# Kernel optimization log

Measured on AMD Instinct MI355X. Metric: run time of the kernel, lower is better.

The kernel has to match this reference:

```python
import jax, jax.numpy as jnp
import numpy as np

D_MODEL = 1024
NUM_HEADS = 16
HEAD_DIM = D_MODEL // NUM_HEADS
SEQ_LEN = 2048
BATCH = 2


def setup_inputs() -> dict:
    key = jax.random.key(0)
    ks = jax.random.split(key, 8)
    s = 1.0 / np.sqrt(D_MODEL)
    x = jax.random.normal(ks[0], (BATCH, SEQ_LEN, D_MODEL), jnp.float32)
    Wq = jax.random.normal(ks[1], (D_MODEL, D_MODEL), jnp.float32) * s
    Wk = jax.random.normal(ks[2], (D_MODEL, D_MODEL), jnp.float32) * s
    Wv = jax.random.normal(ks[3], (D_MODEL, D_MODEL), jnp.float32) * s
    Wo = jax.random.normal(ks[4], (D_MODEL, D_MODEL), jnp.float32) * s
    bq = jnp.zeros((D_MODEL,), jnp.float32)
    bk = jnp.zeros((D_MODEL,), jnp.float32)
    bv = jnp.zeros((D_MODEL,), jnp.float32)
    bo = jnp.zeros((D_MODEL,), jnp.float32)
    pos_embed = jax.random.normal(ks[5], (SEQ_LEN, HEAD_DIM), jnp.float32) * (1.0 / np.sqrt(HEAD_DIM))
    alpha = jnp.ones((NUM_HEADS, 1, 1), jnp.float32)
    beta = jnp.zeros((NUM_HEADS, 1, 1), jnp.float32)
    mask = jnp.ones((BATCH, SEQ_LEN), jnp.int32)
    return {"x": x, "mask": mask, "Wq": Wq, "bq": bq, "Wk": Wk, "bk": bk,
            "Wv": Wv, "bv": bv, "Wo": Wo, "bo": bo,
            "pos_embed": pos_embed, "alpha": alpha, "beta": beta}


def reference(x, mask, Wq, bq, Wk, bk, Wv, bv, Wo, bo, pos_embed, alpha, beta):
    B, S, _ = x.shape
    H, Dh = NUM_HEADS, HEAD_DIM
    # projections (torch Linear: x @ W^T + b), reshape to [B,H,S,Dh]
    def proj(W, b):
        return (x @ W.T + b).reshape(B, S, H, Dh).transpose(0, 2, 1, 3)
    q = proj(Wq, bq)
    k = proj(Wk, bk)
    v = proj(Wv, bv)
    # content scores [B,H,S,S]
    content = jnp.einsum('bhqd,bhkd->bhqk', q, k) / np.sqrt(Dh).astype(np.float32)
    # position scores [S,S] -> broadcast; combined with per-head alpha/beta
    pe = pos_embed[:S]
    pos_attn = pe @ pe.T  # [S,S]
    scores = content + (alpha * pos_attn[None] + beta)[None]  # [B,H,S,S]
    # mask: [B,S] broadcast over heads and query positions (key-side mask)
    scores = jnp.where(mask[:, None, None, :] == 0, -jnp.inf, scores)
    probs = jax.nn.softmax(scores, axis=-1)
    out = jnp.einsum('bhqk,bhkd->bhqd', probs, v)  # [B,H,S,Dh]
    out = out.transpose(0, 2, 1, 3).reshape(B, S, H * Dh)
    return out @ Wo.T + bo
```

## Files before the change

kernel.cpp:

```cpp
#include <hip/hip_runtime.h>

#define BATCH 2
#define SEQ   2048
#define NH    16
#define DH    64
#define DA    128
#define DM    1024
#define MTOT  (BATCH*SEQ)

typedef _Float16 f16x8 __attribute__((ext_vector_type(8)));
typedef _Float16 f16x4 __attribute__((ext_vector_type(4)));
typedef float    f32x4 __attribute__((ext_vector_type(4)));
typedef float    f32x16 __attribute__((ext_vector_type(16)));

#define LOG2E 1.44269504088896340736f

#define OFF_X16 0u
#define OFF_WQ  8388608u
#define OFF_WK  10485760u
#define OFF_WV  12582912u
#define OFF_WO  14680064u
#define OFF_QA  16777216u
#define OFF_KA  33554432u
#define OFF_VT  50331648u
#define OFF_AO  58720256u

__device__ __forceinline__ void gload_lds16(const _Float16* g, _Float16* l) {
  __builtin_amdgcn_global_load_lds(
      (const __attribute__((address_space(1))) unsigned int*)g,
      (__attribute__((address_space(3))) unsigned int*)l, 16, 0, 0);
}

__device__ __forceinline__ float fexp2(float x) {
  float r;
  asm("v_exp_f32 %0, %1" : "=v"(r) : "v"(x));
  return r;
}

__device__ __forceinline__ unsigned pk2(float a, float b) {
  auto v = __builtin_amdgcn_cvt_pkrtz(a, b);
  return *(unsigned*)&v;
}

__global__ __launch_bounds__(256) void cvt_all(
    const float* __restrict__ x,  const float* __restrict__ wq,
    const float* __restrict__ wk, const float* __restrict__ wv,
    const float* __restrict__ wo, _Float16* __restrict__ dst)
{
  int i = blockIdx.x * 256 + threadIdx.x;
  const float* src;
  if (i < 524288) {
    src = x + (size_t)i * 8;
  } else {
    int j = i - 524288;
    int wi = j >> 17;
    const float* w = (wi == 0) ? wq : ((wi == 1) ? wk : ((wi == 2) ? wv : wo));
    src = w + (size_t)(j & 131071) * 8;
  }
  float4 a = ((const float4*)src)[0];
  float4 c = ((const float4*)src)[1];
  f16x8 hv;
  hv[0]=(_Float16)a.x; hv[1]=(_Float16)a.y; hv[2]=(_Float16)a.z; hv[3]=(_Float16)a.w;
  hv[4]=(_Float16)c.x; hv[5]=(_Float16)c.y; hv[6]=(_Float16)c.z; hv[7]=(_Float16)c.w;
  *(f16x8*)(dst + (size_t)i * 8) = hv;
}

__global__ __launch_bounds__(256) void fill_pe(
    const float* __restrict__ pe, const float* __restrict__ alpha,
    _Float16* __restrict__ Qa, _Float16* __restrict__ Ka)
{
  int idx = blockIdx.x * 256 + threadIdx.x;
  int c8 = idx & 7;
  int s  = (idx >> 3) & 2047;
  int h  = (idx >> 14) & 15;
  int b  = idx >> 18;
  const float4* p4 = (const float4*)(pe + s * 64 + c8 * 8);
  float4 a = p4[0], c = p4[1];
  float al = alpha[h] * LOG2E;
  f16x8 hk, hq;
  hk[0]=(_Float16)a.x; hk[1]=(_Float16)a.y; hk[2]=(_Float16)a.z; hk[3]=(_Float16)a.w;
  hk[4]=(_Float16)c.x; hk[5]=(_Float16)c.y; hk[6]=(_Float16)c.z; hk[7]=(_Float16)c.w;
  hq[0]=(_Float16)(al*a.x); hq[1]=(_Float16)(al*a.y); hq[2]=(_Float16)(al*a.z); hq[3]=(_Float16)(al*a.w);
  hq[4]=(_Float16)(al*c.x); hq[5]=(_Float16)(al*c.y); hq[6]=(_Float16)(al*c.z); hq[7]=(_Float16)(al*c.w);
  size_t o = ((size_t)((b * NH + h) * SEQ + s)) * DA + 64 + c8 * 8;
  *(f16x8*)&Qa[o] = hq;
  *(f16x8*)&Ka[o] = hk;
}

template<int MODE>
__global__ __launch_bounds__(256) void gemm_nt(
    const _Float16* __restrict__ A,
    const _Float16* __restrict__ W0, const _Float16* __restrict__ W1,
    const _Float16* __restrict__ W2,
    const float* __restrict__ b0, const float* __restrict__ b1,
    const float* __restrict__ b2,
    _Float16* __restrict__ Qa, _Float16* __restrict__ Ka,
    _Float16* __restrict__ Vt, float* __restrict__ Out)
{
  __shared__ _Float16 As[128 * 64];
  __shared__ _Float16 Bs[128 * 64];
  const int tid = threadIdx.x;
  const int w = tid >> 6, lane = tid & 63;
  const int g = lane >> 4, l16 = lane & 15;
  const int wm = w >> 1, wn = w & 1;

  int nb_all = blockIdx.x;
  int mblk = blockIdx.y;
  const _Float16* Bp; const float* biasp;
  int which = 0, nblk = nb_all;
  if (MODE == 0) {
    which = nb_all >> 3; nblk = nb_all & 7;
    Bp = (which == 0) ? W0 : ((which == 1) ? W1 : W2);
    biasp = (which == 0) ? b0 : ((which == 1) ? b1 : b2);
  } else {
    Bp = W0; biasp = b0;
  }

  f32x4 zero4 = {0.f, 0.f, 0.f, 0.f};
  f32x4 acc[4][4];
  #pragma unroll
  for (int mb = 0; mb < 4; ++mb)
    #pragma unroll
    for (int nb = 0; nb < 4; ++nb) acc[mb][nb] = zero4;

  const _Float16* Abase = A  + (size_t)mblk * 128 * DM;
  const _Float16* Bbase = Bp + (size_t)nblk * 128 * DM;

  for (int kt = 0; kt < DM / 64; ++kt) {
    __syncthreads();
    #pragma unroll
    for (int ii = 0; ii < 4; ++ii) {
      int i = w * 4 + ii;
      int rt = i * 8 + (lane >> 3);
      int cg = (lane & 7) ^ (rt & 7);
      gload_lds16(Abase + (size_t)rt * DM + kt * 64 + cg * 8, &As[i * 512]);
    }
    #pragma unroll
    for (int ii = 0; ii < 4; ++ii) {
      int i = w * 4 + ii;
      int rt = i * 8 + (lane >> 3);
      int cg = (lane & 7) ^ (rt & 7);
      gload_lds16(Bbase + (size_t)rt * DM + kt * 64 + cg * 8, &Bs[i * 512]);
    }
    __syncthreads();
    #pragma unroll
    for (int ks = 0; ks < 2; ++ks) {
      f16x8 av[4], bv[4];
      #pragma unroll
      for (int mb = 0; mb < 4; ++mb) {
        int rt = wm * 64 + mb * 16 + l16;
        av[mb] = *(const f16x8*)&As[rt * 64 + (((ks * 4 + g) ^ (rt & 7)) * 8)];
      }
      #pragma unroll
      for (int nb = 0; nb < 4; ++nb) {
        int rt = wn * 64 + nb * 16 + l16;
        bv[nb] = *(const f16x8*)&Bs[rt * 64 + (((ks * 4 + g) ^ (rt & 7)) * 8)];
      }
      #pragma unroll
      for (int mb = 0; mb < 4; ++mb)
        #pragma unroll
        for (int nb = 0; nb < 4; ++nb)
          acc[mb][nb] = __builtin_amdgcn_mfma_f32_16x16x32_f16(
              av[mb], bv[nb], acc[mb][nb], 0, 0, 0);
    }
  }

  #pragma unroll
  for (int nb = 0; nb < 4; ++nb) {
    int n = nblk * 128 + wn * 64 + nb * 16 + l16;
    float bias = biasp[n];
    #pragma unroll
    for (int mb = 0; mb < 4; ++mb) {
      int m0 = mblk * 128 + wm * 64 + mb * 16 + g * 4;
      if (MODE == 0) {
        int hh = n >> 6, dd = n & 63;
        if (which == 2) {
          int bb = m0 >> 11, ss = m0 & 2047;
          f16x4 hv;
          #pragma unroll
          for (int r = 0; r < 4; ++r) hv[r] = (_Float16)(acc[mb][nb][r] + bias);
          *(f16x4*)&Vt[((size_t)((bb * NH + hh) * DH + dd)) * SEQ + ss] = hv;
        } else {
          #pragma unroll
          for (int r = 0; r < 4; ++r) {
            int m = m0 + r; int bb = m >> 11, ss = m & 2047;
            size_t o = ((size_t)((bb * NH + hh) * SEQ + ss)) * DA + dd;
            if (which == 0) Qa[o] = (_Float16)((acc[mb][nb][r] + bias) * (0.125f * LOG2E));
            else            Ka[o] = (_Float16)(acc[mb][nb][r] + bias);
          }
        }
      } else {
        #pragma unroll
        for (int r = 0; r < 4; ++r)
          Out[(size_t)(m0 + r) * DM + n] = acc[mb][nb][r] + bias;
      }
    }
  }
}

__global__ __launch_bounds__(256, 3) void flash_attn(
    const _Float16* __restrict__ Qa, const _Float16* __restrict__ Ka,
    const _Float16* __restrict__ Vt, const int* __restrict__ mask,
    _Float16* __restrict__ AO)
{
  __shared__ _Float16 Ks[2][64 * 128];
  __shared__ _Float16 Vs[2][64 * 64];
  const int tid = threadIdx.x;
  const int w = tid >> 6, lane = tid & 63;
  const int l32 = lane & 31, hi = lane >> 5;

  int bid = blockIdx.x;
  int work = (bid & 7) * 64 + (bid >> 3);
  const int qt = work & 15;
  const int bh = work >> 4;
  const int h = bh & 15, b = bh >> 4;

  const _Float16* qbase = Qa + ((size_t)(bh * SEQ) + qt * 128 + w * 32) * DA;
  f16x8 qf[8];
  #pragma unroll
  for (int c16 = 0; c16 < 8; ++c16)
    qf[c16] = *(const f16x8*)&qbase[l32 * DA + c16 * 16 + hi * 8];

  f32x16 acco[2];
  #pragma unroll
  for (int db = 0; db < 2; ++db)
    #pragma unroll
    for (int r = 0; r < 16; ++r) acco[db][r] = 0.f;
  float mrun = -3.0e38f, lrun = 0.f;

  const _Float16* kbase = Ka + (size_t)bh * SEQ * DA;
  const _Float16* vbase = Vt + (size_t)bh * DH * SEQ;
  const int* mbase = mask + b * SEQ;

  int allm = 1;
  #pragma unroll 8
  for (int t = 0; t < SEQ / 64; ++t) allm &= (mbase[t * 64 + lane] != 0);
  const bool maskclean = __all(allm);

  auto STAGE = [&](int buf, int kt) {
    #pragma unroll
    for (int ii = 0; ii < 4; ++ii) {
      int i = ii * 256 + tid;
      int rt = i >> 4, c = i & 15;
      int cg = c ^ (rt & 7);
      gload_lds16(kbase + (size_t)(kt * 64 + rt) * DA + cg * 8, &Ks[buf][i * 8]);
    }
    #pragma unroll
    for (int ii = 0; ii < 2; ++ii) {
      int i = ii * 256 + tid;
      int rt = i >> 3, c = i & 7;
      int cg = c ^ (rt & 7);
      gload_lds16(vbase + (size_t)rt * SEQ + kt * 64 + cg * 8, &Vs[buf][i * 8]);
    }
  };

  STAGE(0, 0);
  int cur = 0;
  for (int kt = 0; kt < SEQ / 64; ++kt) {
    asm volatile("s_waitcnt lgkmcnt(0)" ::: "memory");
    __builtin_amdgcn_s_barrier();
    asm volatile("" ::: "memory");
    if (kt + 1 < SEQ / 64) {
      STAGE(cur ^ 1, kt + 1);
      asm volatile("s_waitcnt vmcnt(6)" ::: "memory");
    } else {
      asm volatile("s_waitcnt vmcnt(0)" ::: "memory");
    }
    __builtin_amdgcn_s_barrier();
    asm volatile("" ::: "memory");

    f32x16 sfr[2];
    __builtin_amdgcn_s_setprio(1);
    #pragma unroll
    for (int kb = 0; kb < 2; ++kb) {
      f32x16 s;
      #pragma unroll
      for (int r = 0; r < 16; ++r) s[r] = 0.f;
      int rt = kb * 32 + l32;
      #pragma unroll
      for (int c16 = 0; c16 < 8; ++c16) {
        int ch = (2 * c16 + hi) ^ (rt & 7);
        f16x8 kf = *(const f16x8*)&Ks[cur][rt * 128 + ch * 8];
        s = __builtin_amdgcn_mfma_f32_32x32x16_f16(kf, qf[c16], s, 0, 0, 0);
      }
      sfr[kb] = s;
    }
    __builtin_amdgcn_s_setprio(0);

    if (!maskclean) {
      #pragma unroll
      for (int kb = 0; kb < 2; ++kb)
        #pragma unroll
        for (int r = 0; r < 16; ++r) {
          int key = kt * 64 + kb * 32 + (r & 3) + 8 * (r >> 2) + 4 * hi;
          if (mbase[key] == 0) sfr[kb][r] = -3.0e38f;
        }
    }

    float mx = sfr[0][0];
    #pragma unroll
    for (int kb = 0; kb < 2; ++kb)
      #pragma unroll
      for (int r = 0; r < 16; ++r) mx = fmaxf(mx, sfr[kb][r]);
    mx = fmaxf(mx, __shfl_xor(mx, 32));

    const bool rescale = !__all(mx <= mrun + 8.0f);
    float mnew = mrun, scale = 1.0f;
    if (rescale) {
      mnew = fmaxf(mrun, mx);
      scale = fexp2(mrun - mnew);
    }
    float rsum = 0.f;
    unsigned pk[2][4][2];
    #pragma unroll
    for (int kb = 0; kb < 2; ++kb)
      #pragma unroll
      for (int rq = 0; rq < 4; ++rq) {
        float p0 = fexp2(sfr[kb][rq * 4 + 0] - mnew);
        float p1 = fexp2(sfr[kb][rq * 4 + 1] - mnew);
        float p2 = fexp2(sfr[kb][rq * 4 + 2] - mnew);
        float p3 = fexp2(sfr[kb][rq * 4 + 3] - mnew);
        rsum += (p0 + p1) + (p2 + p3);
        pk[kb][rq][0] = pk2(p0, p1);
        pk[kb][rq][1] = pk2(p2, p3);
      }
    rsum += __shfl_xor(rsum, 32);
    if (rescale) {
      lrun = lrun * scale + rsum;
      mrun = mnew;
      #pragma unroll
      for (int db = 0; db < 2; ++db)
        #pragma unroll
        for (int r = 0; r < 16; ++r) acco[db][r] *= scale;
    } else {
      lrun += rsum;
    }

    __builtin_amdgcn_s_setprio(1);
    #pragma unroll
    for (int c = 0; c < 4; ++c) {
      const int kb = c >> 1, c2 = c & 1;
      unsigned X0 = pk[kb][2 * c2][0],     X1 = pk[kb][2 * c2][1];
      unsigned Y0 = pk[kb][2 * c2 + 1][0], Y1 = pk[kb][2 * c2 + 1][1];
      asm("v_permlane32_swap_b32 %0, %1" : "+v"(X0), "+v"(Y0));
      asm("v_permlane32_swap_b32 %0, %1" : "+v"(X1), "+v"(Y1));
      union { unsigned u[4]; f16x8 v; } pu;
      pu.u[0] = X0; pu.u[1] = X1; pu.u[2] = Y0; pu.u[3] = Y1;
      #pragma unroll
      for (int db = 0; db < 2; ++db) {
        int row = db * 32 + l32;
        int ch = (2 * c + hi) ^ (row & 7);
        f16x8 vf = *(const f16x8*)&Vs[cur][row * 64 + ch * 8];
        acco[db] = __builtin_amdgcn_mfma_f32_32x32x16_f16(vf, pu.v, acco[db], 0, 0, 0);
      }
    }
    __builtin_amdgcn_s_setprio(0);
    cur ^= 1;
  }

  float inv = 1.0f / lrun;
  int sg = qt * 128 + w * 32 + l32;
  _Float16* aobase = AO + ((size_t)(b * SEQ + sg)) * DM + h * DH;
  #pragma unroll
  for (int db = 0; db < 2; ++db)
    #pragma unroll
    for (int rq = 0; rq < 4; ++rq) {
      f16x4 o;
      #pragma unroll
      for (int j = 0; j < 4; ++j) o[j] = (_Float16)(acco[db][rq * 4 + j] * inv);
      *(f16x4*)&aobase[db * 32 + rq * 8 + hi * 4] = o;
    }
}

extern "C" void kernel_launch(void* const* d_in, const int* in_sizes, int n_in,
                              void* d_out, int out_size, void* d_ws, size_t ws_size,
                              hipStream_t stream) {
  const float* x     = (const float*)d_in[0];
  const int*   mask  = (const int*)  d_in[1];
  const float* Wq    = (const float*)d_in[2];
  const float* bq    = (const float*)d_in[3];
  const float* Wk    = (const float*)d_in[4];
  const float* bk    = (const float*)d_in[5];
  const float* Wv    = (const float*)d_in[6];
  const float* bv    = (const float*)d_in[7];
  const float* Wo    = (const float*)d_in[8];
  const float* bo    = (const float*)d_in[9];
  const float* pe    = (const float*)d_in[10];
  const float* alpha = (const float*)d_in[11];

  char* ws = (char*)d_ws;
  _Float16* x16 = (_Float16*)(ws + OFF_X16);
  _Float16* wq6 = (_Float16*)(ws + OFF_WQ);
  _Float16* wk6 = (_Float16*)(ws + OFF_WK);
  _Float16* wv6 = (_Float16*)(ws + OFF_WV);
  _Float16* wo6 = (_Float16*)(ws + OFF_WO);
  _Float16* Qa  = (_Float16*)(ws + OFF_QA);
  _Float16* Ka  = (_Float16*)(ws + OFF_KA);
  _Float16* Vt  = (_Float16*)(ws + OFF_VT);
  _Float16* AO  = (_Float16*)(ws + OFF_AO);
  float* out = (float*)d_out;

  cvt_all<<<4096, 256, 0, stream>>>(x, Wq, Wk, Wv, Wo, x16);
  fill_pe<<<2048, 256, 0, stream>>>(pe, alpha, Qa, Ka);
  gemm_nt<0><<<dim3(24, 32), 256, 0, stream>>>(x16, wq6, wk6, wv6, bq, bk, bv,
                                               Qa, Ka, Vt, nullptr);
  flash_attn<<<512, 256, 0, stream>>>(Qa, Ka, Vt, mask, AO);
  gemm_nt<1><<<dim3(8, 32), 256, 0, stream>>>(AO, wo6, nullptr, nullptr, bo,
                                              nullptr, nullptr, nullptr, nullptr,
                                              nullptr, out);
}
```

Measured before the change: 149.4 us.

## Split online softmax into per-32-key sub-blocks interleaved with PV MFMAs

Restructures the attention inner loop so the max/rescale/exp/PV-MFMA sequence runs separately for each 32-key half of the 64-key tile, instead of once over the whole tile. This lets the softmax VALU work of one half overlap with the MFMAs of the other and lowers register pressure, since only one half's packed probabilities are live at a time. In exchange there are twice as many cross-lane reductions and rescale checks per tile, so the accumulator may be rescaled more often.

Measured after the change: 154.7 us. +3.5%, slower.

```diff
diff --git a/kernel.cpp b/kernel.cpp
--- a/kernel.cpp
+++ b/kernel.cpp
@@ -287,74 +287,68 @@
     }
     __builtin_amdgcn_s_setprio(0);
 
-    if (!maskclean) {
-      #pragma unroll
-      for (int kb = 0; kb < 2; ++kb)
+    #pragma unroll
+    for (int kb = 0; kb < 2; ++kb) {
+      if (!maskclean) {
         #pragma unroll
         for (int r = 0; r < 16; ++r) {
           int key = kt * 64 + kb * 32 + (r & 3) + 8 * (r >> 2) + 4 * hi;
           if (mbase[key] == 0) sfr[kb][r] = -3.0e38f;
         }
-    }
-
-    float mx = sfr[0][0];
-    #pragma unroll
-    for (int kb = 0; kb < 2; ++kb)
-      #pragma unroll
-      for (int r = 0; r < 16; ++r) mx = fmaxf(mx, sfr[kb][r]);
-    mx = fmaxf(mx, __shfl_xor(mx, 32));
-
-    const bool rescale = !__all(mx <= mrun + 8.0f);
-    float mnew = mrun, scale = 1.0f;
-    if (rescale) {
-      mnew = fmaxf(mrun, mx);
-      scale = fexp2(mrun - mnew);
-    }
-    float rsum = 0.f;
-    unsigned pk[2][4][2];
-    #pragma unroll
-    for (int kb = 0; kb < 2; ++kb)
+      }
+      float t0 = fmaxf(fmaxf(sfr[kb][0], sfr[kb][1]), fmaxf(sfr[kb][2], sfr[kb][3]));
+      float t1 = fmaxf(fmaxf(sfr[kb][4], sfr[kb][5]), fmaxf(sfr[kb][6], sfr[kb][7]));
+      float t2 = fmaxf(fmaxf(sfr[kb][8], sfr[kb][9]), fmaxf(sfr[kb][10], sfr[kb][11]));
+      float t3 = fmaxf(fmaxf(sfr[kb][12], sfr[kb][13]), fmaxf(sfr[kb][14], sfr[kb][15]));
+      float mx = fmaxf(fmaxf(t0, t1), fmaxf(t2, t3));
+      mx = fmaxf(mx, __shfl_xor(mx, 32));
+
+      const bool rescale = !__all(mx <= mrun + 8.0f);
+      if (rescale) {
+        float mnew = fmaxf(mrun, mx);
+        float scale = fexp2(mrun - mnew);
+        lrun *= scale;
+        #pragma unroll
+        for (int db = 0; db < 2; ++db)
+          #pragma unroll
+          for (int r = 0; r < 16; ++r) acco[db][r] *= scale;
+        mrun = mnew;
+      }
+      float rsum = 0.f;
+      unsigned pk[4][2];
       #pragma unroll
       for (int rq = 0; rq < 4; ++rq) {
-        float p0 = fexp2(sfr[kb][rq * 4 + 0] - mnew);
-        float p1 = fexp2(sfr[kb][rq * 4 + 1] - mnew);
-        float p2 = fexp2(sfr[kb][rq * 4 + 2] - mnew);
-        float p3 = fexp2(sfr[kb][rq * 4 + 3] - mnew);
+        float p0 = fexp2(sfr[kb][rq * 4 + 0] - mrun);
+        float p1 = fexp2(sfr[kb][rq * 4 + 1] - mrun);
+        float p2 = fexp2(sfr[kb][rq * 4 + 2] - mrun);
+        float p3 = fexp2(sfr[kb][rq * 4 + 3] - mrun);
         rsum += (p0 + p1) + (p2 + p3);
-        pk[kb][rq][0] = pk2(p0, p1);
-        pk[kb][rq][1] = pk2(p2, p3);
-      }
-    rsum += __shfl_xor(rsum, 32);
-    if (rescale) {
-      lrun = lrun * scale + rsum;
-      mrun = mnew;
-      #pragma unroll
-      for (int db = 0; db < 2; ++db)
+        pk[rq][0] = pk2(p0, p1);
+        pk[rq][1] = pk2(p2, p3);
+      }
+      rsum += __shfl_xor(rsum, 32);
+      lrun += rsum;
+
+      __builtin_amdgcn_s_setprio(1);
+      #pragma unroll
+      for (int c2 = 0; c2 < 2; ++c2) {
+        unsigned X0 = pk[2 * c2][0],     X1 = pk[2 * c2][1];
+        unsigned Y0 = pk[2 * c2 + 1][0], Y1 = pk[2 * c2 + 1][1];
+        asm("v_permlane32_swap_b32 %0, %1" : "+v"(X0), "+v"(Y0));
+        asm("v_permlane32_swap_b32 %0, %1" : "+v"(X1), "+v"(Y1));
+        union { unsigned u[4]; f16x8 v; } pu;
+        pu.u[0] = X0; pu.u[1] = X1; pu.u[2] = Y0; pu.u[3] = Y1;
+        const int c = kb * 2 + c2;
         #pragma unroll
-        for (int r = 0; r < 16; ++r) acco[db][r] *= scale;
-    } else {
-      lrun += rsum;
-    }
-
-    __builtin_amdgcn_s_setprio(1);
-    #pragma unroll
-    for (int c = 0; c < 4; ++c) {
-      const int kb = c >> 1, c2 = c & 1;
-      unsigned X0 = pk[kb][2 * c2][0],     X1 = pk[kb][2 * c2][1];
-      unsigned Y0 = pk[kb][2 * c2 + 1][0], Y1 = pk[kb][2 * c2 + 1][1];
-      asm("v_permlane32_swap_b32 %0, %1" : "+v"(X0), "+v"(Y0));
-      asm("v_permlane32_swap_b32 %0, %1" : "+v"(X1), "+v"(Y1));
-      union { unsigned u[4]; f16x8 v; } pu;
-      pu.u[0] = X0; pu.u[1] = X1; pu.u[2] = Y0; pu.u[3] = Y1;
-      #pragma unroll
-      for (int db = 0; db < 2; ++db) {
-        int row = db * 32 + l32;
-        int ch = (2 * c + hi) ^ (row & 7);
-        f16x8 vf = *(const f16x8*)&Vs[cur][row * 64 + ch * 8];
-        acco[db] = __builtin_amdgcn_mfma_f32_32x32x16_f16(vf, pu.v, acco[db], 0, 0, 0);
-      }
-    }
-    __builtin_amdgcn_s_setprio(0);
+        for (int db = 0; db < 2; ++db) {
+          int row = db * 32 + l32;
+          int ch = (2 * c + hi) ^ (row & 7);
+          f16x8 vf = *(const f16x8*)&Vs[cur][row * 64 + ch * 8];
+          acco[db] = __builtin_amdgcn_mfma_f32_32x32x16_f16(vf, pu.v, acco[db], 0, 0, 0);
+        }
+      }
+      __builtin_amdgcn_s_setprio(0);
+    }
     cur ^= 1;
   }
 
```

## Split attention keys across two halves and merge partials in a combine kernel

Applied to the files above, without the earlier changes.

The flash-attention kernel now gives each 512-thread block 256 queries (8 waves) over one half of the keys. It writes normalized fp16 partial outputs plus per-row (max, sum) statistics, and a new combine_halves kernel merges the two halves with log-sum-exp weights. The wider block shares each staged K/V tile across twice as many query waves, which halves global-to-LDS staging per query, and each block loop is half as long. In exchange it adds an extra kernel launch, extra partial-output traffic, and reuses dead workspace regions (x16, the Wq area) as scratch. It also tightens launch bounds to (512,4), which may force register spills given the large per-thread accumulator and fragment state.

Measured after the change: 156.7 us. 4.9% more time.

```diff
diff --git a/kernel.cpp b/kernel.cpp
--- a/kernel.cpp
+++ b/kernel.cpp
@@ -198,10 +198,11 @@
   }
 }
 
-__global__ __launch_bounds__(256, 3) void flash_attn(
+__global__ __launch_bounds__(512, 4) void flash_attn(
     const _Float16* __restrict__ Qa, const _Float16* __restrict__ Ka,
     const _Float16* __restrict__ Vt, const int* __restrict__ mask,
-    _Float16* __restrict__ AO)
+    _Float16* __restrict__ pp0, _Float16* __restrict__ pp1,
+    float2* __restrict__ Ml)
 {
   __shared__ _Float16 Ks[2][64 * 128];
   __shared__ _Float16 Vs[2][64 * 64];
@@ -211,11 +212,12 @@
 
   int bid = blockIdx.x;
   int work = (bid & 7) * 64 + (bid >> 3);
-  const int qt = work & 15;
-  const int bh = work >> 4;
+  const int qt   = work & 7;
+  const int half = (work >> 3) & 1;
+  const int bh   = work >> 4;
   const int h = bh & 15, b = bh >> 4;
 
-  const _Float16* qbase = Qa + ((size_t)(bh * SEQ) + qt * 128 + w * 32) * DA;
+  const _Float16* qbase = Qa + ((size_t)(bh * SEQ) + qt * 256 + w * 32) * DA;
   f16x8 qf[8];
   #pragma unroll
   for (int c16 = 0; c16 < 8; ++c16)
@@ -226,28 +228,27 @@
   for (int db = 0; db < 2; ++db)
     #pragma unroll
     for (int r = 0; r < 16; ++r) acco[db][r] = 0.f;
-  float mrun = -3.0e38f, lrun = 0.f;
-
-  const _Float16* kbase = Ka + (size_t)bh * SEQ * DA;
-  const _Float16* vbase = Vt + (size_t)bh * DH * SEQ;
-  const int* mbase = mask + b * SEQ;
+  float mrun = -1.0e30f, lrun = 0.f;
+
+  const _Float16* kbase = Ka + (size_t)bh * SEQ * DA + (size_t)half * 1024 * DA;
+  const _Float16* vbase = Vt + (size_t)bh * DH * SEQ + half * 1024;
+  const int* mbase = mask + b * SEQ + half * 1024;
 
   int allm = 1;
   #pragma unroll 8
-  for (int t = 0; t < SEQ / 64; ++t) allm &= (mbase[t * 64 + lane] != 0);
+  for (int t = 0; t < 16; ++t) allm &= (mbase[t * 64 + lane] != 0);
   const bool maskclean = __all(allm);
 
   auto STAGE = [&](int buf, int kt) {
     #pragma unroll
-    for (int ii = 0; ii < 4; ++ii) {
-      int i = ii * 256 + tid;
+    for (int ii = 0; ii < 2; ++ii) {
+      int i = ii * 512 + tid;
       int rt = i >> 4, c = i & 15;
       int cg = c ^ (rt & 7);
       gload_lds16(kbase + (size_t)(kt * 64 + rt) * DA + cg * 8, &Ks[buf][i * 8]);
     }
-    #pragma unroll
-    for (int ii = 0; ii < 2; ++ii) {
-      int i = ii * 256 + tid;
+    {
+      int i = tid;
       int rt = i >> 3, c = i & 7;
       int cg = c ^ (rt & 7);
       gload_lds16(vbase + (size_t)rt * SEQ + kt * 64 + cg * 8, &Vs[buf][i * 8]);
@@ -256,13 +257,13 @@
 
   STAGE(0, 0);
   int cur = 0;
-  for (int kt = 0; kt < SEQ / 64; ++kt) {
+  for (int kt = 0; kt < 16; ++kt) {
     asm volatile("s_waitcnt lgkmcnt(0)" ::: "memory");
     __builtin_amdgcn_s_barrier();
     asm volatile("" ::: "memory");
-    if (kt + 1 < SEQ / 64) {
+    if (kt + 1 < 16) {
       STAGE(cur ^ 1, kt + 1);
-      asm volatile("s_waitcnt vmcnt(6)" ::: "memory");
+      asm volatile("s_waitcnt vmcnt(3)" ::: "memory");
     } else {
       asm volatile("s_waitcnt vmcnt(0)" ::: "memory");
     }
@@ -297,11 +298,16 @@
         }
     }
 
-    float mx = sfr[0][0];
-    #pragma unroll
-    for (int kb = 0; kb < 2; ++kb)
-      #pragma unroll
-      for (int r = 0; r < 16; ++r) mx = fmaxf(mx, sfr[kb][r]);
+    float t0 = fmaxf(fmaxf(sfr[0][0], sfr[0][1]), fmaxf(sfr[0][2], sfr[0][3]));
+    float t1 = fmaxf(fmaxf(sfr[0][4], sfr[0][5]), fmaxf(sfr[0][6], sfr[0][7]));
+    float t2 = fmaxf(fmaxf(sfr[0][8], sfr[0][9]), fmaxf(sfr[0][10], sfr[0][11]));
+    float t3 = fmaxf(fmaxf(sfr[0][12], sfr[0][13]), fmaxf(sfr[0][14], sfr[0][15]));
+    float u0 = fmaxf(fmaxf(sfr[1][0], sfr[1][1]), fmaxf(sfr[1][2], sfr[1][3]));
+    float u1 = fmaxf(fmaxf(sfr[1][4], sfr[1][5]), fmaxf(sfr[1][6], sfr[1][7]));
+    float u2 = fmaxf(fmaxf(sfr[1][8], sfr[1][9]), fmaxf(sfr[1][10], sfr[1][11]));
+    float u3 = fmaxf(fmaxf(sfr[1][12], sfr[1][13]), fmaxf(sfr[1][14], sfr[1][15]));
+    float mx = fmaxf(fmaxf(fmaxf(t0, t1), fmaxf(t2, t3)),
+                     fmaxf(fmaxf(u0, u1), fmaxf(u2, u3)));
     mx = fmaxf(mx, __shfl_xor(mx, 32));
 
     const bool rescale = !__all(mx <= mrun + 8.0f);
@@ -358,9 +364,9 @@
     cur ^= 1;
   }
 
-  float inv = 1.0f / lrun;
-  int sg = qt * 128 + w * 32 + l32;
-  _Float16* aobase = AO + ((size_t)(b * SEQ + sg)) * DM + h * DH;
+  float inv = (lrun > 0.f) ? (1.0f / lrun) : 0.f;
+  int sg = qt * 256 + w * 32 + l32;
+  _Float16* pb = (half ? pp1 : pp0) + ((size_t)(b * SEQ + sg)) * DM + h * DH;
   #pragma unroll
   for (int db = 0; db < 2; ++db)
     #pragma unroll
@@ -368,8 +374,39 @@
       f16x4 o;
       #pragma unroll
       for (int j = 0; j < 4; ++j) o[j] = (_Float16)(acco[db][rq * 4 + j] * inv);
-      *(f16x4*)&aobase[db * 32 + rq * 8 + hi * 4] = o;
-    }
+      *(f16x4*)&pb[db * 32 + rq * 8 + hi * 4] = o;
+    }
+  if (hi == 0) {
+    float2 ml; ml.x = mrun; ml.y = lrun;
+    Ml[((size_t)half * 32 + bh) * SEQ + sg] = ml;
+  }
+}
+
+__global__ __launch_bounds__(256) void combine_halves(
+    const _Float16* __restrict__ pp0, const _Float16* pp1,
+    const float2* __restrict__ Ml, _Float16* AO)
+{
+  int idx = blockIdx.x * 256 + threadIdx.x;
+  int d8 = idx & 7;
+  int h  = (idx >> 3) & 15;
+  int s  = (idx >> 7) & 2047;
+  int b  = idx >> 18;
+  int bh = b * NH + h;
+  float2 ml0 = Ml[(size_t)bh * SEQ + s];
+  float2 ml1 = Ml[((size_t)32 + bh) * SEQ + s];
+  float m = fmaxf(ml0.x, ml1.x);
+  float w0 = fexp2(ml0.x - m) * ml0.y;
+  float w1 = fexp2(ml1.x - m) * ml1.y;
+  float inv = 1.0f / (w0 + w1);
+  w0 *= inv; w1 *= inv;
+  size_t off = ((size_t)(b * SEQ + s)) * DM + h * DH + d8 * 8;
+  f16x8 a = *(const f16x8*)&pp0[off];
+  f16x8 c = *(const f16x8*)&pp1[off];
+  f16x8 o;
+  #pragma unroll
+  for (int j = 0; j < 8; ++j)
+    o[j] = (_Float16)(w0 * (float)a[j] + w1 * (float)c[j]);
+  *(f16x8*)&AO[off] = o;
 }
 
 extern "C" void kernel_launch(void* const* d_in, const int* in_sizes, int n_in,
@@ -398,13 +435,15 @@
   _Float16* Ka  = (_Float16*)(ws + OFF_KA);
   _Float16* Vt  = (_Float16*)(ws + OFF_VT);
   _Float16* AO  = (_Float16*)(ws + OFF_AO);
+  float2*   Ml  = (float2*)(ws + OFF_WQ);
   float* out = (float*)d_out;
 
   cvt_all<<<4096, 256, 0, stream>>>(x, Wq, Wk, Wv, Wo, x16);
   fill_pe<<<2048, 256, 0, stream>>>(pe, alpha, Qa, Ka);
   gemm_nt<0><<<dim3(24, 32), 256, 0, stream>>>(x16, wq6, wk6, wv6, bq, bk, bv,
                                                Qa, Ka, Vt, nullptr);
-  flash_attn<<<512, 256, 0, stream>>>(Qa, Ka, Vt, mask, AO);
+  flash_attn<<<512, 512, 0, stream>>>(Qa, Ka, Vt, mask, x16, AO, Ml);
+  combine_halves<<<2048, 256, 0, stream>>>(x16, AO, Ml, AO);
   gemm_nt<1><<<dim3(8, 32), 256, 0, stream>>>(AO, wo6, nullptr, nullptr, bo,
                                               nullptr, nullptr, nullptr, nullptr,
                                               nullptr, out);
```

## Software-pipeline flash attention: overlap QK of next tile with softmax/PV

Applied to the files above, without the earlier changes.

Restructures the flash-attention main loop so the QK^T MFMAs for key tile t are issued in the same step as the softmax and PV MFMAs for tile t-1, ping-ponging two score register sets. V staging becomes triple-buffered so the PV of the previous tile can read while the next tile is loaded. The point is to hide softmax latency behind matrix work. In exchange it uses more registers and LDS, and launch bounds drop from 3 to 2 blocks per CU, which lowers occupancy. It also reshapes the max reduction into a tree, changes the running-max initial value, and guards the final 1/l division.

Measured after the change: 153.5 us. 2.8% more time.

```diff
diff --git a/kernel.cpp b/kernel.cpp
--- a/kernel.cpp
+++ b/kernel.cpp
@@ -198,13 +198,13 @@
   }
 }
 
-__global__ __launch_bounds__(256, 3) void flash_attn(
+__global__ __launch_bounds__(256, 2) void flash_attn(
     const _Float16* __restrict__ Qa, const _Float16* __restrict__ Ka,
     const _Float16* __restrict__ Vt, const int* __restrict__ mask,
     _Float16* __restrict__ AO)
 {
   __shared__ _Float16 Ks[2][64 * 128];
-  __shared__ _Float16 Vs[2][64 * 64];
+  __shared__ _Float16 Vs[3][64 * 64];
   const int tid = threadIdx.x;
   const int w = tid >> 6, lane = tid & 63;
   const int l32 = lane & 31, hi = lane >> 5;
@@ -226,7 +226,7 @@
   for (int db = 0; db < 2; ++db)
     #pragma unroll
     for (int r = 0; r < 16; ++r) acco[db][r] = 0.f;
-  float mrun = -3.0e38f, lrun = 0.f;
+  float mrun = -1.0e30f, lrun = 0.f;
 
   const _Float16* kbase = Ka + (size_t)bh * SEQ * DA;
   const _Float16* vbase = Vt + (size_t)bh * DH * SEQ;
@@ -237,39 +237,27 @@
   for (int t = 0; t < SEQ / 64; ++t) allm &= (mbase[t * 64 + lane] != 0);
   const bool maskclean = __all(allm);
 
-  auto STAGE = [&](int buf, int kt) {
+  auto STAGE = [&](int kt) {
+    _Float16* kd = &Ks[kt & 1][0];
+    _Float16* vd = &Vs[kt % 3][0];
     #pragma unroll
     for (int ii = 0; ii < 4; ++ii) {
       int i = ii * 256 + tid;
       int rt = i >> 4, c = i & 15;
       int cg = c ^ (rt & 7);
-      gload_lds16(kbase + (size_t)(kt * 64 + rt) * DA + cg * 8, &Ks[buf][i * 8]);
+      gload_lds16(kbase + (size_t)(kt * 64 + rt) * DA + cg * 8, kd + i * 8);
     }
     #pragma unroll
     for (int ii = 0; ii < 2; ++ii) {
       int i = ii * 256 + tid;
       int rt = i >> 3, c = i & 7;
       int cg = c ^ (rt & 7);
-      gload_lds16(vbase + (size_t)rt * SEQ + kt * 64 + cg * 8, &Vs[buf][i * 8]);
+      gload_lds16(vbase + (size_t)rt * SEQ + kt * 64 + cg * 8, vd + i * 8);
     }
   };
 
-  STAGE(0, 0);
-  int cur = 0;
-  for (int kt = 0; kt < SEQ / 64; ++kt) {
-    asm volatile("s_waitcnt lgkmcnt(0)" ::: "memory");
-    __builtin_amdgcn_s_barrier();
-    asm volatile("" ::: "memory");
-    if (kt + 1 < SEQ / 64) {
-      STAGE(cur ^ 1, kt + 1);
-      asm volatile("s_waitcnt vmcnt(6)" ::: "memory");
-    } else {
-      asm volatile("s_waitcnt vmcnt(0)" ::: "memory");
-    }
-    __builtin_amdgcn_s_barrier();
-    asm volatile("" ::: "memory");
-
-    f32x16 sfr[2];
+  auto QK = [&](f32x16 (&sfr)[2], int kt) {
+    const _Float16* kd = &Ks[kt & 1][0];
     __builtin_amdgcn_s_setprio(1);
     #pragma unroll
     for (int kb = 0; kb < 2; ++kb) {
@@ -280,13 +268,16 @@
       #pragma unroll
       for (int c16 = 0; c16 < 8; ++c16) {
         int ch = (2 * c16 + hi) ^ (rt & 7);
-        f16x8 kf = *(const f16x8*)&Ks[cur][rt * 128 + ch * 8];
+        f16x8 kf = *(const f16x8*)&kd[rt * 128 + ch * 8];
         s = __builtin_amdgcn_mfma_f32_32x32x16_f16(kf, qf[c16], s, 0, 0, 0);
       }
       sfr[kb] = s;
     }
     __builtin_amdgcn_s_setprio(0);
-
+  };
+
+  auto SMPV = [&](f32x16 (&sfr)[2], int kt) {
+    const _Float16* vd = &Vs[kt % 3][0];
     if (!maskclean) {
       #pragma unroll
       for (int kb = 0; kb < 2; ++kb)
@@ -296,12 +287,16 @@
           if (mbase[key] == 0) sfr[kb][r] = -3.0e38f;
         }
     }
-
-    float mx = sfr[0][0];
-    #pragma unroll
-    for (int kb = 0; kb < 2; ++kb)
-      #pragma unroll
-      for (int r = 0; r < 16; ++r) mx = fmaxf(mx, sfr[kb][r]);
+    float t0 = fmaxf(fmaxf(sfr[0][0], sfr[0][1]), fmaxf(sfr[0][2], sfr[0][3]));
+    float t1 = fmaxf(fmaxf(sfr[0][4], sfr[0][5]), fmaxf(sfr[0][6], sfr[0][7]));
+    float t2 = fmaxf(fmaxf(sfr[0][8], sfr[0][9]), fmaxf(sfr[0][10], sfr[0][11]));
+    float t3 = fmaxf(fmaxf(sfr[0][12], sfr[0][13]), fmaxf(sfr[0][14], sfr[0][15]));
+    float u0 = fmaxf(fmaxf(sfr[1][0], sfr[1][1]), fmaxf(sfr[1][2], sfr[1][3]));
+    float u1 = fmaxf(fmaxf(sfr[1][4], sfr[1][5]), fmaxf(sfr[1][6], sfr[1][7]));
+    float u2 = fmaxf(fmaxf(sfr[1][8], sfr[1][9]), fmaxf(sfr[1][10], sfr[1][11]));
+    float u3 = fmaxf(fmaxf(sfr[1][12], sfr[1][13]), fmaxf(sfr[1][14], sfr[1][15]));
+    float mx = fmaxf(fmaxf(fmaxf(t0, t1), fmaxf(t2, t3)),
+                     fmaxf(fmaxf(u0, u1), fmaxf(u2, u3)));
     mx = fmaxf(mx, __shfl_xor(mx, 32));
 
     const bool rescale = !__all(mx <= mrun + 8.0f);
@@ -335,7 +330,6 @@
     } else {
       lrun += rsum;
     }
-
     __builtin_amdgcn_s_setprio(1);
     #pragma unroll
     for (int c = 0; c < 4; ++c) {
@@ -350,15 +344,45 @@
       for (int db = 0; db < 2; ++db) {
         int row = db * 32 + l32;
         int ch = (2 * c + hi) ^ (row & 7);
-        f16x8 vf = *(const f16x8*)&Vs[cur][row * 64 + ch * 8];
+        f16x8 vf = *(const f16x8*)&vd[row * 64 + ch * 8];
         acco[db] = __builtin_amdgcn_mfma_f32_32x32x16_f16(vf, pu.v, acco[db], 0, 0, 0);
       }
     }
     __builtin_amdgcn_s_setprio(0);
-    cur ^= 1;
+  };
+
+  auto HALF = [&](f32x16 (&sc)[2], f32x16 (&sp)[2], int t) {
+    asm volatile("s_waitcnt lgkmcnt(0)" ::: "memory");
+    __builtin_amdgcn_s_barrier();
+    asm volatile("" ::: "memory");
+    if (t + 1 < SEQ / 64) {
+      STAGE(t + 1);
+      asm volatile("s_waitcnt vmcnt(6)" ::: "memory");
+    } else {
+      asm volatile("s_waitcnt vmcnt(0)" ::: "memory");
+    }
+    __builtin_amdgcn_s_barrier();
+    asm volatile("" ::: "memory");
+    QK(sc, t);
+    SMPV(sp, t - 1);
+  };
+
+  f32x16 sA[2], sB[2];
+  STAGE(0);
+  STAGE(1);
+  asm volatile("s_waitcnt vmcnt(6)" ::: "memory");
+  __builtin_amdgcn_s_barrier();
+  asm volatile("" ::: "memory");
+  QK(sA, 0);
+
+  for (int t = 1; t < SEQ / 64; t += 2) {
+    HALF(sB, sA, t);
+    if (t + 1 < SEQ / 64)
+      HALF(sA, sB, t + 1);
   }
-
-  float inv = 1.0f / lrun;
+  SMPV(sB, SEQ / 64 - 1);
+
+  float inv = (lrun > 0.f) ? (1.0f / lrun) : 0.f;
   int sg = qt * 128 + w * 32 + l32;
   _Float16* aobase = AO + ((size_t)(b * SEQ + sg)) * DM + h * DH;
   #pragma unroll
```
